# Optimization experiments

Measured on AMD Instinct MI355X. Metric: run time of the kernel, lower is better.

The kernel has to match this reference:

```python
import jax, jax.numpy as jnp
import numpy as np

N_V, N_E = 4096, 16384
IN_V, OUT_V, IN_E = 128, 128, 64


def setup_inputs() -> dict:
    key = jax.random.key(0)
    k1, k2, k3, k4, k5, k6, k7 = jax.random.split(key, 7)
    stdv = 1.0 / np.sqrt(OUT_V)
    return {
        "H_v": jax.random.normal(k1, (N_V, IN_V), dtype=jnp.float32),
        "H_e": jax.random.normal(k2, (N_E, IN_E), dtype=jnp.float32),
        "adj_e": jnp.zeros((1, 1), dtype=jnp.float32),  # unused in node_layer branch
        "adj_v": jax.random.uniform(k3, (N_V, N_V), dtype=jnp.float32),
        "T": jax.random.uniform(k4, (N_V, N_E), dtype=jnp.float32),
        "weight": jax.random.uniform(k5, (IN_V, OUT_V), minval=-stdv, maxval=stdv, dtype=jnp.float32),
        "p": jax.random.normal(k6, (1, IN_E), dtype=jnp.float32),
        "bias": jax.random.uniform(k7, (OUT_V,), minval=-stdv, maxval=stdv, dtype=jnp.float32),
    }


def reference(H_v, H_e, adj_e, adj_v, T, weight, p, bias):
    # node_layer=True branch of AlternateConvolution.forward
    # diag((H_e @ p.T).T[0]) -> per-edge scalar; T @ diag(d) == column-scale T
    diag_vals = (H_e @ p.T)[:, 0]                      # [n_e]
    multiplier1 = (T * diag_vals[None, :]) @ T.T       # [n_v, n_v]
    eye = jnp.eye(multiplier1.shape[0], dtype=multiplier1.dtype)
    M1 = eye + (1.0 - eye) * multiplier1               # diagonal forced to 1
    adjusted_A = M1 * adj_v                            # elementwise adjacency mask
    ret = adjusted_A @ (H_v @ weight) + bias           # [n_v, out_v]
    return (ret, H_e)
```

## Files before the change

### kernel.cpp

```cpp
#include <hip/hip_runtime.h>
#include <stdint.h>


typedef __attribute__((ext_vector_type(4))) float floatx4;
typedef __attribute__((ext_vector_type(4))) int intx4;
typedef __attribute__((ext_vector_type(8))) short short8;
typedef __attribute__((ext_vector_type(4))) unsigned short u16x4;

#define AS1 __attribute__((address_space(1)))
#define AS3 __attribute__((address_space(3)))

__device__ __forceinline__ void gload_lds16(const void* g, void* l) {
  __builtin_amdgcn_global_load_lds(
      (const AS1 unsigned int*)(uintptr_t)g,
      (AS3 unsigned int*)(uint32_t)(uintptr_t)l, 16, 0, 0);
}

__device__ __forceinline__ unsigned short f32_to_bf16(float f) {
  union { float f; unsigned int u; } v;
  v.f = f;
  unsigned int r = 0x7fffu + ((v.u >> 16) & 1u);
  return (unsigned short)((v.u + r) >> 16);
}

__device__ __forceinline__ float bf16_to_f32(unsigned short s) {
  union { unsigned int u; float f; } cv;
  cv.u = (unsigned int)s << 16;
  return cv.f;
}

__device__ __forceinline__ void tri_decode(int t, int& bi, int& bj) {
  bi = 0;
  while (t >= 32 - bi) { t -= 32 - bi; ++bi; }
  bj = bi + t;
}

#define TA_SCALE 3.96875f
#define DEQ_SCALE (32.0f / 16129.0f)

__global__ __launch_bounds__(256) void edge_dot_kernel(
    const float* __restrict__ He, const float* __restrict__ p,
    float* __restrict__ dvals) {
  int e = blockIdx.x * 4 + (threadIdx.x >> 6);
  int lane = threadIdx.x & 63;
  float v = He[e * 64 + lane] * p[lane];
#pragma unroll
  for (int off = 32; off > 0; off >>= 1) v += __shfl_down(v, off);
  if (lane == 0) dvals[e] = v;
}

__global__ __launch_bounds__(256) void copy4_kernel(
    const floatx4* __restrict__ src, floatx4* __restrict__ dst, int n4) {
  int i = blockIdx.x * 256 + threadIdx.x;
  if (i < n4)
    __builtin_nontemporal_store(__builtin_nontemporal_load(src + i), dst + i);
}

__global__ __launch_bounds__(256) void convert_T_i8_kernel(
    const floatx4* __restrict__ T4, const float* __restrict__ dvals,
    uint2* __restrict__ Ta8, uint2* __restrict__ Tb8) {
  int i = blockIdx.x * 256 + threadIdx.x;
  floatx4 t0 = __builtin_nontemporal_load(T4 + 2 * i);
  floatx4 t1 = __builtin_nontemporal_load(T4 + 2 * i + 1);
  int col = (i << 3) & 16383;
  const floatx4* dv = (const floatx4*)(dvals + col);
  floatx4 d0 = dv[0], d1 = dv[1];
  union { signed char c[8]; uint2 u; } qa, qb;
#pragma unroll
  for (int q = 0; q < 4; ++q) {
    float sa0 = fminf(fmaxf(t0[q] * d0[q] * TA_SCALE, -127.f), 127.f);
    float sa1 = fminf(fmaxf(t1[q] * d1[q] * TA_SCALE, -127.f), 127.f);
    qa.c[q]     = (signed char)(int)rintf(sa0);
    qa.c[q + 4] = (signed char)(int)rintf(sa1);
    qb.c[q]     = (signed char)(int)rintf(t0[q] * 127.0f);
    qb.c[q + 4] = (signed char)(int)rintf(t1[q] * 127.0f);
  }
  Ta8[i] = qa.u;
  Tb8[i] = qb.u;
}

__global__ __launch_bounds__(256) void hwt_kernel(
    const float* __restrict__ Hv, const float* __restrict__ W,
    unsigned short* __restrict__ HWT) {
  int idx = blockIdx.x * 256 + threadIdx.x;
  int j = idx & 4095, o = idx >> 12;
  float s = 0.f;
#pragma unroll 8
  for (int c = 0; c < 128; ++c) s += Hv[j * 128 + c] * W[c * 128 + o];
  HWT[o * 4096 + j] = f32_to_bf16(s);
}

__global__ __launch_bounds__(256) void gemm1_split_kernel(
    const signed char* __restrict__ Ta, const signed char* __restrict__ Tb,
    int* __restrict__ part) {
  constexpr int K = 16384;
  __shared__ __align__(16) signed char As[128 * 128];
  __shared__ __align__(16) signed char Bs[128 * 128];

  const int d = blockIdx.x;
  const int rank = (d & 7) * 132 + (d >> 3);
  const int h = rank >= 528 ? 1 : 0;
  const int t = rank - h * 528;
  int bi, bj;
  tri_decode(t, bi, bj);

  const int tid = threadIdx.x;
  const int wave = tid >> 6, lane = tid & 63;
  const int wr = (wave >> 1) * 64, wc = (wave & 1) * 64;
  const int quad = lane >> 4, mrow = lane & 15;

  const int srow = tid >> 3;
  const int cg = (tid & 7) ^ (srow & 7);
  const signed char* Ag = Ta + (size_t)(bi * 128 + srow) * K + cg * 16;
  const signed char* Bg = Tb + (size_t)(bj * 128 + srow) * K + cg * 16;

  intx4 acc[4][4] = {};

  const int kbeg = h * 8192, kend = kbeg + 8192;
  for (int k0 = kbeg; k0 < kend; k0 += 128) {
    __syncthreads();
#pragma unroll
    for (int q = 0; q < 4; ++q) {
      gload_lds16(Ag + (size_t)(q * 32) * K + k0, As + q * 4096 + tid * 16);
      gload_lds16(Bg + (size_t)(q * 32) * K + k0, Bs + q * 4096 + tid * 16);
    }
    __syncthreads();

#pragma unroll
    for (int sk = 0; sk < 2; ++sk) {
      intx4 af[4], bf[4];
#pragma unroll
      for (int x = 0; x < 4; ++x) {
        const int ra = wr + x * 16 + mrow;
        const int rb = wc + x * 16 + mrow;
        af[x] = *(const intx4*)&As[ra * 128 + (((sk * 4 + quad) ^ (ra & 7))) * 16];
        bf[x] = *(const intx4*)&Bs[rb * 128 + (((sk * 4 + quad) ^ (rb & 7))) * 16];
      }
#pragma unroll
      for (int tr = 0; tr < 4; ++tr)
#pragma unroll
        for (int tc = 0; tc < 4; ++tc)
          acc[tr][tc] = __builtin_amdgcn_mfma_i32_16x16x64_i8(
              af[tr], bf[tc], acc[tr][tc], 0, 0, 0);
    }
  }

  int* pt = part + ((size_t)h * 528 + t) * 16384;
#pragma unroll
  for (int tr = 0; tr < 4; ++tr) {
    const int rbase = wr + tr * 16 + quad * 4;
#pragma unroll
    for (int tc = 0; tc < 4; ++tc) {
      const int col = wc + tc * 16 + mrow;
#pragma unroll
      for (int r = 0; r < 4; ++r)
        __builtin_nontemporal_store(acc[tr][tc][r],
                                    &pt[(rbase + r) * 128 + col]);
    }
  }
}

__global__ __launch_bounds__(256) void combine_kernel(
    const int* __restrict__ part, const float* __restrict__ adj_v,
    unsigned short* __restrict__ adjA) {
  constexpr int NV = 4096;
  __shared__ unsigned short mt[128 * 68];

  const int b = blockIdx.x;
  const int t = b >> 1, r0 = (b & 1) * 64;
  int bi, bj;
  tri_decode(t, bi, bj);
  const int tid = threadIdx.x;
  const bool diag = (bi == bj);

  const int* pt0 = part + (size_t)t * 16384;
  const int* pt1 = pt0 + (size_t)528 * 16384;

#pragma unroll
  for (int j = 0; j < 8; ++j) {
    const int e = j * 1024 + tid * 4;
    const int row = r0 + (e >> 7);
    const int col = e & 127;
    intx4 a = __builtin_nontemporal_load((const intx4*)(pt0 + row * 128 + col));
    intx4 c = __builtin_nontemporal_load((const intx4*)(pt1 + row * 128 + col));
    floatx4 msk = __builtin_nontemporal_load(
        (const floatx4*)(adj_v + (size_t)(bi * 128 + row) * NV + bj * 128 + col));
    u16x4 o;
#pragma unroll
    for (int q = 0; q < 4; ++q) {
      float m = (float)(a[q] + c[q]) * DEQ_SCALE;
      float val = (diag && row == col + q) ? msk[q] : m * msk[q];
      ((unsigned short*)&o)[q] = f32_to_bf16(val);
      if (!diag) mt[(col + q) * 68 + (row - r0)] = f32_to_bf16(m);
    }
    *(u16x4*)(adjA + (size_t)(bi * 128 + row) * NV + bj * 128 + col) = o;
  }

  if (diag) return;
  __syncthreads();

#pragma unroll
  for (int j = 0; j < 8; ++j) {
    const int e = j * 1024 + tid * 4;
    const int mc = e >> 6;
    const int mr = e & 63;
    u16x4 mv = *(const u16x4*)&mt[mc * 68 + mr];
    floatx4 msk = __builtin_nontemporal_load(
        (const floatx4*)(adj_v + (size_t)(bj * 128 + mc) * NV + bi * 128 + r0 + mr));
    u16x4 o;
#pragma unroll
    for (int q = 0; q < 4; ++q)
      ((unsigned short*)&o)[q] =
          f32_to_bf16(bf16_to_f32(((const unsigned short*)&mv)[q]) * msk[q]);
    *(u16x4*)(adjA + (size_t)(bj * 128 + mc) * NV + bi * 128 + r0 + mr) = o;
  }
}

__global__ __launch_bounds__(256) void gemm2_kernel(
    const unsigned short* __restrict__ adjA, const unsigned short* __restrict__ HWT,
    float* __restrict__ gpart) {
  constexpr int K = 4096, OUTV = 128;
  __shared__ __align__(16) unsigned short As[128 * 32];
  __shared__ __align__(16) unsigned short Bs[128 * 32];

  const int tid = threadIdx.x;
  const int wave = tid >> 6, lane = tid & 63;
  const int bi = blockIdx.x, ks = blockIdx.y;
  const int wr = (wave >> 1) * 64, wc = (wave & 1) * 64;
  const int quad = lane >> 4, mrow = lane & 15;

  const int sr = tid >> 2, sc = (tid & 3) * 8;
  const unsigned short* Ag = adjA + (size_t)(bi * 128 + sr) * K + sc;
  const unsigned short* Bg = HWT + (size_t)sr * K + sc;

  floatx4 acc[4][4] = {};

  const int kbeg = ks * 512, kend = kbeg + 512;
  for (int k0 = kbeg; k0 < kend; k0 += 32) {
    __syncthreads();
    gload_lds16(Ag + k0, &As[tid * 8]);
    gload_lds16(Ag + (size_t)64 * K + k0, &As[tid * 8 + 2048]);
    gload_lds16(Bg + k0, &Bs[tid * 8]);
    gload_lds16(Bg + (size_t)64 * K + k0, &Bs[tid * 8 + 2048]);
    __syncthreads();

    short8 af[4], bf[4];
#pragma unroll
    for (int x = 0; x < 4; ++x) {
      af[x] = *(const short8*)&As[(wr + x * 16 + mrow) * 32 + quad * 8];
      bf[x] = *(const short8*)&Bs[(wc + x * 16 + mrow) * 32 + quad * 8];
    }
#pragma unroll
    for (int tr = 0; tr < 4; ++tr)
#pragma unroll
      for (int tc = 0; tc < 4; ++tc)
        acc[tr][tc] = __builtin_amdgcn_mfma_f32_16x16x32_bf16(
            af[tr], bf[tc], acc[tr][tc], 0, 0, 0);
  }

#pragma unroll
  for (int tr = 0; tr < 4; ++tr) {
    const int rbase = bi * 128 + wr + tr * 16 + quad * 4;
#pragma unroll
    for (int tc = 0; tc < 4; ++tc) {
      const int col = wc + tc * 16 + mrow;
#pragma unroll
      for (int r = 0; r < 4; ++r)
        gpart[(size_t)ks * 524288 + (size_t)(rbase + r) * OUTV + col] =
            acc[tr][tc][r];
    }
  }
}

__global__ __launch_bounds__(256) void reduce_bias_kernel(
    const float* __restrict__ gpart, const float* __restrict__ bias,
    float* __restrict__ out) {
  int i = blockIdx.x * 256 + threadIdx.x;
  floatx4 acc = *(const floatx4*)&bias[(i & 31) * 4];
#pragma unroll
  for (int ks = 0; ks < 8; ++ks)
    acc += __builtin_nontemporal_load((const floatx4*)gpart +
                                      (size_t)ks * 131072 + i);
  __builtin_nontemporal_store(acc, (floatx4*)out + i);
}

extern "C" void kernel_launch(void* const* d_in, const int* in_sizes, int n_in,
                              void* d_out, int out_size, void* d_ws, size_t ws_size,
                              hipStream_t stream) {
  const float* H_v    = (const float*)d_in[0];
  const float* H_e    = (const float*)d_in[1];
  const float* adj_v  = (const float*)d_in[3];
  const float* T      = (const float*)d_in[4];
  const float* weight = (const float*)d_in[5];
  const float* p      = (const float*)d_in[6];
  const float* bias   = (const float*)d_in[7];
  float* out = (float*)d_out;

  char* ws = (char*)d_ws;
  signed char* Ta      = (signed char*)(ws);
  signed char* Tb      = (signed char*)(ws + 67108864);
  int* part            = (int*)(ws + 134217728);
  unsigned short* adjA = (unsigned short*)(ws + 203423744);
  unsigned short* HWT  = (unsigned short*)(ws + 236978176);
  float* dvals         = (float*)(ws + 238026752);
  float* gpart         = (float*)(ws + 238092288);

  edge_dot_kernel<<<dim3(4096), dim3(256), 0, stream>>>(H_e, p, dvals);
  copy4_kernel<<<dim3(1024), dim3(256), 0, stream>>>(
      (const floatx4*)H_e, (floatx4*)(out + 524288), 262144);
  hwt_kernel<<<dim3(2048), dim3(256), 0, stream>>>(H_v, weight, HWT);

  convert_T_i8_kernel<<<dim3(32768), dim3(256), 0, stream>>>(
      (const floatx4*)T, dvals, (uint2*)Ta, (uint2*)Tb);

  gemm1_split_kernel<<<dim3(1056), dim3(256), 0, stream>>>(Ta, Tb, part);
  combine_kernel<<<dim3(1056), dim3(256), 0, stream>>>(part, adj_v, adjA);

  gemm2_kernel<<<dim3(32, 8), dim3(256), 0, stream>>>(adjA, HWT, gpart);
  reduce_bias_kernel<<<dim3(512), dim3(256), 0, stream>>>(gpart, bias, out);
}
```

Before: 652.5 us.

## Double-buffer LDS in both GEMMs and switch int8 GEMM to 32x32 MFMA

```diff
diff --git a/kernel.cpp b/kernel.cpp
--- a/kernel.cpp
+++ b/kernel.cpp
@@ -4,6 +4,7 @@
 
 typedef __attribute__((ext_vector_type(4))) float floatx4;
 typedef __attribute__((ext_vector_type(4))) int intx4;
+typedef __attribute__((ext_vector_type(16))) int intx16;
 typedef __attribute__((ext_vector_type(8))) short short8;
 typedef __attribute__((ext_vector_type(4))) unsigned short u16x4;
 
@@ -94,8 +95,8 @@
     const signed char* __restrict__ Ta, const signed char* __restrict__ Tb,
     int* __restrict__ part) {
   constexpr int K = 16384;
-  __shared__ __align__(16) signed char As[128 * 128];
-  __shared__ __align__(16) signed char Bs[128 * 128];
+  __shared__ __align__(16) signed char As[2][128 * 128];
+  __shared__ __align__(16) signed char Bs[2][128 * 128];
 
   const int d = blockIdx.x;
   const int rank = (d & 7) * 132 + (d >> 3);
@@ -107,57 +108,72 @@
   const int tid = threadIdx.x;
   const int wave = tid >> 6, lane = tid & 63;
   const int wr = (wave >> 1) * 64, wc = (wave & 1) * 64;
-  const int quad = lane >> 4, mrow = lane & 15;
+  const int row32 = lane & 31, khalf = lane >> 5;
 
   const int srow = tid >> 3;
   const int cg = (tid & 7) ^ (srow & 7);
   const signed char* Ag = Ta + (size_t)(bi * 128 + srow) * K + cg * 16;
   const signed char* Bg = Tb + (size_t)(bj * 128 + srow) * K + cg * 16;
 
-  intx4 acc[4][4] = {};
+  intx16 acc[2][2] = {};
 
   const int kbeg = h * 8192, kend = kbeg + 8192;
-  for (int k0 = kbeg; k0 < kend; k0 += 128) {
+
+  auto stage = [&](int b, int k0) {
+#pragma unroll
+    for (int q = 0; q < 4; ++q) {
+      gload_lds16(Ag + (size_t)(q * 32) * K + k0, &As[b][q * 4096 + tid * 16]);
+      gload_lds16(Bg + (size_t)(q * 32) * K + k0, &Bs[b][q * 4096 + tid * 16]);
+    }
+  };
+
+  auto compute = [&](int b) {
+    intx4 af[2][4], bf[2][4];
+#pragma unroll
+    for (int x = 0; x < 2; ++x) {
+      const int ra = wr + x * 32 + row32;
+      const int rb = wc + x * 32 + row32;
+#pragma unroll
+      for (int sk = 0; sk < 4; ++sk) {
+        af[x][sk] =
+            *(const intx4*)&As[b][ra * 128 + ((sk * 2 + khalf) ^ (ra & 7)) * 16];
+        bf[x][sk] =
+            *(const intx4*)&Bs[b][rb * 128 + ((sk * 2 + khalf) ^ (rb & 7)) * 16];
+      }
+    }
+#pragma unroll
+    for (int sk = 0; sk < 4; ++sk)
+#pragma unroll
+      for (int tr = 0; tr < 2; ++tr)
+#pragma unroll
+        for (int tc = 0; tc < 2; ++tc)
+          acc[tr][tc] = __builtin_amdgcn_mfma_i32_32x32x32_i8(
+              af[tr][sk], bf[tc][sk], acc[tr][tc], 0, 0, 0);
+  };
+
+  stage(0, kbeg);
+  __syncthreads();
+  int buf = 0;
+  for (int k0 = kbeg; k0 < kend - 128; k0 += 128) {
+    stage(buf ^ 1, k0 + 128);
+    compute(buf);
     __syncthreads();
-#pragma unroll
-    for (int q = 0; q < 4; ++q) {
-      gload_lds16(Ag + (size_t)(q * 32) * K + k0, As + q * 4096 + tid * 16);
-      gload_lds16(Bg + (size_t)(q * 32) * K + k0, Bs + q * 4096 + tid * 16);
-    }
-    __syncthreads();
-
-#pragma unroll
-    for (int sk = 0; sk < 2; ++sk) {
-      intx4 af[4], bf[4];
-#pragma unroll
-      for (int x = 0; x < 4; ++x) {
-        const int ra = wr + x * 16 + mrow;
-        const int rb = wc + x * 16 + mrow;
-        af[x] = *(const intx4*)&As[ra * 128 + (((sk * 4 + quad) ^ (ra & 7))) * 16];
-        bf[x] = *(const intx4*)&Bs[rb * 128 + (((sk * 4 + quad) ^ (rb & 7))) * 16];
+    buf ^= 1;
+  }
+  compute(buf);
+
+  int* pt = part + ((size_t)h * 528 + t) * 16384;
+#pragma unroll
+  for (int tr = 0; tr < 2; ++tr)
+#pragma unroll
+    for (int tc = 0; tc < 2; ++tc) {
+      const int col = wc + tc * 32 + row32;
+#pragma unroll
+      for (int r = 0; r < 16; ++r) {
+        const int row = wr + tr * 32 + (r & 3) + 8 * (r >> 2) + 4 * khalf;
+        __builtin_nontemporal_store(acc[tr][tc][r], &pt[row * 128 + col]);
       }
-#pragma unroll
-      for (int tr = 0; tr < 4; ++tr)
-#pragma unroll
-        for (int tc = 0; tc < 4; ++tc)
-          acc[tr][tc] = __builtin_amdgcn_mfma_i32_16x16x64_i8(
-              af[tr], bf[tc], acc[tr][tc], 0, 0, 0);
-    }
-  }
-
-  int* pt = part + ((size_t)h * 528 + t) * 16384;
-#pragma unroll
-  for (int tr = 0; tr < 4; ++tr) {
-    const int rbase = wr + tr * 16 + quad * 4;
-#pragma unroll
-    for (int tc = 0; tc < 4; ++tc) {
-      const int col = wc + tc * 16 + mrow;
-#pragma unroll
-      for (int r = 0; r < 4; ++r)
-        __builtin_nontemporal_store(acc[tr][tc][r],
-                                    &pt[(rbase + r) * 128 + col]);
-    }
-  }
+    }
 }
 
 __global__ __launch_bounds__(256) void combine_kernel(
@@ -220,8 +236,8 @@
     const unsigned short* __restrict__ adjA, const unsigned short* __restrict__ HWT,
     float* __restrict__ gpart) {
   constexpr int K = 4096, OUTV = 128;
-  __shared__ __align__(16) unsigned short As[128 * 32];
-  __shared__ __align__(16) unsigned short Bs[128 * 32];
+  __shared__ __align__(16) unsigned short As[2][128 * 32];
+  __shared__ __align__(16) unsigned short Bs[2][128 * 32];
 
   const int tid = threadIdx.x;
   const int wave = tid >> 6, lane = tid & 63;
@@ -236,19 +252,20 @@
   floatx4 acc[4][4] = {};
 
   const int kbeg = ks * 512, kend = kbeg + 512;
-  for (int k0 = kbeg; k0 < kend; k0 += 32) {
-    __syncthreads();
-    gload_lds16(Ag + k0, &As[tid * 8]);
-    gload_lds16(Ag + (size_t)64 * K + k0, &As[tid * 8 + 2048]);
-    gload_lds16(Bg + k0, &Bs[tid * 8]);
-    gload_lds16(Bg + (size_t)64 * K + k0, &Bs[tid * 8 + 2048]);
-    __syncthreads();
-
+
+  auto stage = [&](int b, int k0) {
+    gload_lds16(Ag + k0, &As[b][tid * 8]);
+    gload_lds16(Ag + (size_t)64 * K + k0, &As[b][tid * 8 + 2048]);
+    gload_lds16(Bg + k0, &Bs[b][tid * 8]);
+    gload_lds16(Bg + (size_t)64 * K + k0, &Bs[b][tid * 8 + 2048]);
+  };
+
+  auto compute = [&](int b) {
     short8 af[4], bf[4];
 #pragma unroll
     for (int x = 0; x < 4; ++x) {
-      af[x] = *(const short8*)&As[(wr + x * 16 + mrow) * 32 + quad * 8];
-      bf[x] = *(const short8*)&Bs[(wc + x * 16 + mrow) * 32 + quad * 8];
+      af[x] = *(const short8*)&As[b][(wr + x * 16 + mrow) * 32 + quad * 8];
+      bf[x] = *(const short8*)&Bs[b][(wc + x * 16 + mrow) * 32 + quad * 8];
     }
 #pragma unroll
     for (int tr = 0; tr < 4; ++tr)
@@ -256,7 +273,18 @@
       for (int tc = 0; tc < 4; ++tc)
         acc[tr][tc] = __builtin_amdgcn_mfma_f32_16x16x32_bf16(
             af[tr], bf[tc], acc[tr][tc], 0, 0, 0);
-  }
+  };
+
+  stage(0, kbeg);
+  __syncthreads();
+  int buf = 0;
+  for (int k0 = kbeg; k0 < kend - 32; k0 += 32) {
+    stage(buf ^ 1, k0 + 32);
+    compute(buf);
+    __syncthreads();
+    buf ^= 1;
+  }
+  compute(buf);
 
 #pragma unroll
   for (int tr = 0; tr < 4; ++tr) {
```

Result: no change. 663.0 us (+1.6%).

## Fuse int8 gemm1 with combine epilogue and tile the H_v@W kernel

Applied to the files above, without the earlier changes.

```diff
diff --git a/kernel.cpp b/kernel.cpp
--- a/kernel.cpp
+++ b/kernel.cpp
@@ -3,9 +3,11 @@
 
 
 typedef __attribute__((ext_vector_type(4))) float floatx4;
+typedef __attribute__((ext_vector_type(2))) float floatx2;
 typedef __attribute__((ext_vector_type(4))) int intx4;
 typedef __attribute__((ext_vector_type(8))) short short8;
 typedef __attribute__((ext_vector_type(4))) unsigned short u16x4;
+typedef __attribute__((ext_vector_type(2))) unsigned short u16x2;
 
 #define AS1 __attribute__((address_space(1)))
 #define AS3 __attribute__((address_space(3)))
@@ -82,25 +84,48 @@
 __global__ __launch_bounds__(256) void hwt_kernel(
     const float* __restrict__ Hv, const float* __restrict__ W,
     unsigned short* __restrict__ HWT) {
-  int idx = blockIdx.x * 256 + threadIdx.x;
-  int j = idx & 4095, o = idx >> 12;
-  float s = 0.f;
-#pragma unroll 8
-  for (int c = 0; c < 128; ++c) s += Hv[j * 128 + c] * W[c * 128 + o];
-  HWT[o * 4096 + j] = f32_to_bf16(s);
-}
-
-__global__ __launch_bounds__(256) void gemm1_split_kernel(
+  __shared__ float Ws[128 * 128];
+  __shared__ float Hs[32 * 132];
+  const int tid = threadIdx.x;
+#pragma unroll
+  for (int i = 0; i < 16; ++i) {
+    const int g = i * 1024 + tid * 4;
+    *(floatx4*)&Ws[g] = *(const floatx4*)&W[g];
+  }
+  const int j0 = blockIdx.x * 32;
+#pragma unroll
+  for (int i = 0; i < 4; ++i) {
+    const int g = i * 1024 + tid * 4;
+    *(floatx4*)&Hs[(g >> 7) * 132 + (g & 127)] =
+        *(const floatx4*)&Hv[j0 * 128 + g];
+  }
+  __syncthreads();
+  const int j = tid >> 3, l7 = tid & 7;
+  floatx4 acc[4] = {};
+  for (int c = 0; c < 128; ++c) {
+    const float h = Hs[j * 132 + c];
+#pragma unroll
+    for (int m = 0; m < 4; ++m)
+      acc[m] += h * *(const floatx4*)&Ws[c * 128 + m * 32 + l7 * 4];
+  }
+#pragma unroll
+  for (int m = 0; m < 4; ++m)
+#pragma unroll
+    for (int r = 0; r < 4; ++r)
+      HWT[(size_t)(m * 32 + l7 * 4 + r) * 4096 + j0 + j] = f32_to_bf16(acc[m][r]);
+}
+
+__global__ __launch_bounds__(256) void gemm1_fused_kernel(
     const signed char* __restrict__ Ta, const signed char* __restrict__ Tb,
-    int* __restrict__ part) {
-  constexpr int K = 16384;
-  __shared__ __align__(16) signed char As[128 * 128];
-  __shared__ __align__(16) signed char Bs[128 * 128];
+    const float* __restrict__ adj_v, unsigned short* __restrict__ adjA) {
+  constexpr int K = 16384, NV = 4096;
+  __shared__ __align__(16) signed char smem[128 * 134 * 2];
+  signed char* As = smem;
+  signed char* Bs = smem + 16384;
+  unsigned short* mtile = (unsigned short*)smem;
 
   const int d = blockIdx.x;
-  const int rank = (d & 7) * 132 + (d >> 3);
-  const int h = rank >= 528 ? 1 : 0;
-  const int t = rank - h * 528;
+  const int t = (d & 7) * 66 + (d >> 3);
   int bi, bj;
   tri_decode(t, bi, bj);
 
@@ -116,8 +141,7 @@
 
   intx4 acc[4][4] = {};
 
-  const int kbeg = h * 8192, kend = kbeg + 8192;
-  for (int k0 = kbeg; k0 < kend; k0 += 128) {
+  for (int k0 = 0; k0 < K; k0 += 128) {
     __syncthreads();
 #pragma unroll
     for (int q = 0; q < 4; ++q) {
@@ -145,74 +169,50 @@
     }
   }
 
-  int* pt = part + ((size_t)h * 528 + t) * 16384;
-#pragma unroll
-  for (int tr = 0; tr < 4; ++tr) {
-    const int rbase = wr + tr * 16 + quad * 4;
+  __syncthreads();
+#pragma unroll
+  for (int tr = 0; tr < 4; ++tr)
 #pragma unroll
     for (int tc = 0; tc < 4; ++tc) {
       const int col = wc + tc * 16 + mrow;
 #pragma unroll
-      for (int r = 0; r < 4; ++r)
-        __builtin_nontemporal_store(acc[tr][tc][r],
-                                    &pt[(rbase + r) * 128 + col]);
-    }
-  }
-}
-
-__global__ __launch_bounds__(256) void combine_kernel(
-    const int* __restrict__ part, const float* __restrict__ adj_v,
-    unsigned short* __restrict__ adjA) {
-  constexpr int NV = 4096;
-  __shared__ unsigned short mt[128 * 68];
-
-  const int b = blockIdx.x;
-  const int t = b >> 1, r0 = (b & 1) * 64;
-  int bi, bj;
-  tri_decode(t, bi, bj);
-  const int tid = threadIdx.x;
+      for (int r = 0; r < 4; ++r) {
+        const int row = wr + tr * 16 + quad * 4 + r;
+        mtile[row * 134 + col] =
+            f32_to_bf16((float)acc[tr][tc][r] * DEQ_SCALE);
+      }
+    }
+  __syncthreads();
+
   const bool diag = (bi == bj);
 
-  const int* pt0 = part + (size_t)t * 16384;
-  const int* pt1 = pt0 + (size_t)528 * 16384;
-
-#pragma unroll
-  for (int j = 0; j < 8; ++j) {
+#pragma unroll
+  for (int j = 0; j < 32; ++j) {
+    const int e = j * 512 + tid * 2;
+    const int row = e >> 7, col = e & 127;
+    const float m0 = bf16_to_f32(mtile[row * 134 + col]);
+    const float m1 = bf16_to_f32(mtile[row * 134 + col + 1]);
+    floatx2 msk = __builtin_nontemporal_load(
+        (const floatx2*)(adj_v + (size_t)(bi * 128 + row) * NV + bj * 128 + col));
+    u16x2 o;
+    o[0] = f32_to_bf16((diag && row == col)     ? msk[0] : m0 * msk[0]);
+    o[1] = f32_to_bf16((diag && row == col + 1) ? msk[1] : m1 * msk[1]);
+    *(u16x2*)(adjA + (size_t)(bi * 128 + row) * NV + bj * 128 + col) = o;
+  }
+
+  if (diag) return;
+
+#pragma unroll
+  for (int j = 0; j < 16; ++j) {
     const int e = j * 1024 + tid * 4;
-    const int row = r0 + (e >> 7);
-    const int col = e & 127;
-    intx4 a = __builtin_nontemporal_load((const intx4*)(pt0 + row * 128 + col));
-    intx4 c = __builtin_nontemporal_load((const intx4*)(pt1 + row * 128 + col));
+    const int mc = e >> 7, mr = e & 127;
     floatx4 msk = __builtin_nontemporal_load(
-        (const floatx4*)(adj_v + (size_t)(bi * 128 + row) * NV + bj * 128 + col));
+        (const floatx4*)(adj_v + (size_t)(bj * 128 + mc) * NV + bi * 128 + mr));
     u16x4 o;
 #pragma unroll
-    for (int q = 0; q < 4; ++q) {
-      float m = (float)(a[q] + c[q]) * DEQ_SCALE;
-      float val = (diag && row == col + q) ? msk[q] : m * msk[q];
-      ((unsigned short*)&o)[q] = f32_to_bf16(val);
-      if (!diag) mt[(col + q) * 68 + (row - r0)] = f32_to_bf16(m);
-    }
-    *(u16x4*)(adjA + (size_t)(bi * 128 + row) * NV + bj * 128 + col) = o;
-  }
-
-  if (diag) return;
-  __syncthreads();
-
-#pragma unroll
-  for (int j = 0; j < 8; ++j) {
-    const int e = j * 1024 + tid * 4;
-    const int mc = e >> 6;
-    const int mr = e & 63;
-    u16x4 mv = *(const u16x4*)&mt[mc * 68 + mr];
-    floatx4 msk = __builtin_nontemporal_load(
-        (const floatx4*)(adj_v + (size_t)(bj * 128 + mc) * NV + bi * 128 + r0 + mr));
-    u16x4 o;
-#pragma unroll
     for (int q = 0; q < 4; ++q)
-      ((unsigned short*)&o)[q] =
-          f32_to_bf16(bf16_to_f32(((const unsigned short*)&mv)[q]) * msk[q]);
-    *(u16x4*)(adjA + (size_t)(bj * 128 + mc) * NV + bi * 128 + r0 + mr) = o;
+      o[q] = f32_to_bf16(bf16_to_f32(mtile[(mr + q) * 134 + mc]) * msk[q]);
+    *(u16x4*)(adjA + (size_t)(bj * 128 + mc) * NV + bi * 128 + mr) = o;
   }
 }
 
@@ -299,7 +299,6 @@
   char* ws = (char*)d_ws;
   signed char* Ta      = (signed char*)(ws);
   signed char* Tb      = (signed char*)(ws + 67108864);
-  int* part            = (int*)(ws + 134217728);
   unsigned short* adjA = (unsigned short*)(ws + 203423744);
   unsigned short* HWT  = (unsigned short*)(ws + 236978176);
   float* dvals         = (float*)(ws + 238026752);
@@ -308,13 +307,12 @@
   edge_dot_kernel<<<dim3(4096), dim3(256), 0, stream>>>(H_e, p, dvals);
   copy4_kernel<<<dim3(1024), dim3(256), 0, stream>>>(
       (const floatx4*)H_e, (floatx4*)(out + 524288), 262144);
-  hwt_kernel<<<dim3(2048), dim3(256), 0, stream>>>(H_v, weight, HWT);
+  hwt_kernel<<<dim3(128), dim3(256), 0, stream>>>(H_v, weight, HWT);
 
   convert_T_i8_kernel<<<dim3(32768), dim3(256), 0, stream>>>(
       (const floatx4*)T, dvals, (uint2*)Ta, (uint2*)Tb);
 
-  gemm1_split_kernel<<<dim3(1056), dim3(256), 0, stream>>>(Ta, Tb, part);
-  combine_kernel<<<dim3(1056), dim3(256), 0, stream>>>(part, adj_v, adjA);
+  gemm1_fused_kernel<<<dim3(528), dim3(256), 0, stream>>>(Ta, Tb, adj_v, adjA);
 
   gemm2_kernel<<<dim3(32, 8), dim3(256), 0, stream>>>(adjA, HWT, gpart);
   reduce_bias_kernel<<<dim3(512), dim3(256), 0, stream>>>(gpart, bias, out);
```

New measurement: 684.6 us. +4.9%, slower.
